# Performance work log

Hardware: AMD Instinct MI355X
Metric: run time of the kernel (lower is better)

The kernel has to match this reference:

```python
import jax, jax.numpy as jnp
import numpy as np

GROUP = 64      # int4 quantization group size
QMAX = 7.0      # symmetric int4 grid [-8, 7], scales from max/7
EPS = 1e-6      # RMSNorm epsilon


def fake_quant_int4(t, group=GROUP):
    """Symmetric per-group int4 fake-quantization along the last dim (STE)."""
    shp = t.shape
    g = t.reshape(shp[:-1] + (shp[-1] // group, group))
    s = jnp.maximum(jnp.max(jnp.abs(g), axis=-1, keepdims=True) / QMAX, 1e-8)
    q = jnp.clip(jnp.round(g / s), -8.0, 7.0) * s
    out = g + jax.lax.stop_gradient(q - g)  # straight-through
    return out.reshape(shp)


def rms_norm(x, w):
    var = jnp.mean(jnp.square(x), axis=-1, keepdims=True)
    return x * jax.lax.rsqrt(var + EPS) * w


def apply_rope(x, cos, sin):
    # x: [B,S,H,D]; cos/sin: [S, D//2]; rotate consecutive pairs (complex mult)
    xr = x.reshape(x.shape[:-1] + (x.shape[-1] // 2, 2))
    a, b = xr[..., 0], xr[..., 1]
    c = cos[None, :, None, :]
    s = sin[None, :, None, :]
    out = jnp.stack([a * c - b * s, a * s + b * c], axis=-1)
    return out.reshape(x.shape)


def setup_inputs() -> dict:
    B, S, C, OUT, R, D = 2, 4096, 3072, 9216, 32, 128
    key = jax.random.key(0)
    ks = jax.random.split(key, 6)
    x = jax.random.normal(ks[0], (B, S, C), jnp.float32)
    smooth = jax.random.uniform(ks[1], (C,), jnp.float32, minval=0.5, maxval=1.5)
    weight = jax.random.normal(ks[2], (OUT, C), jnp.float32) * 0.02
    proj_down = jax.random.normal(ks[3], (C, R), jnp.float32) * 0.02
    proj_up = jax.random.normal(ks[4], (OUT, R), jnp.float32) * 0.02
    bias = jax.random.normal(ks[5], (OUT,), jnp.float32) * 0.01
    norm_q_weight = jnp.ones((D,), jnp.float32)
    norm_k_weight = jnp.ones((D,), jnp.float32)
    half = D // 2
    inv_freq = 1.0 / (10000.0 ** (jnp.arange(half, dtype=jnp.float32) / half))
    ang = jnp.arange(S, dtype=jnp.float32)[:, None] * inv_freq[None, :]
    return {
        "x": x, "smooth": smooth, "weight": weight,
        "proj_down": proj_down, "proj_up": proj_up, "bias": bias,
        "norm_q_weight": norm_q_weight, "norm_k_weight": norm_k_weight,
        "freqs_cos": jnp.cos(ang), "freqs_sin": jnp.sin(ang),
    }


def reference(x, smooth, weight, proj_down, proj_up, bias,
              norm_q_weight, norm_k_weight, freqs_cos, freqs_sin):
    B, S, C = x.shape
    OUT = weight.shape[0]
    D = norm_q_weight.shape[0]
    H = (OUT // 3) // D
    # --- svdq_quantize_w4a4_act_fuse_lora: smooth, lora-down, int4 quantize ---
    xs = x.reshape(B * S, C) / smooth                 # smoothed activations
    lora_act = xs @ proj_down                          # [BS, R]
    xq = fake_quant_int4(xs)                           # per-token group-64 int4
    # --- svdq_gemm_w4a4: int4 GEMM + LoRA-up + bias epilogue ---
    wq = fake_quant_int4(weight)                       # per-row group-64 int4
    out = xq @ wq.T + lora_act @ proj_up.T + bias      # [BS, OUT]
    out = out.reshape(B, S, 3, H, D)                   # q,k,v concat order
    q, k, v = out[:, :, 0], out[:, :, 1], out[:, :, 2]
    # --- fused RMSNorm + RoPE epilogue on q and k ---
    q = apply_rope(rms_norm(q, norm_q_weight), freqs_cos, freqs_sin)
    k = apply_rope(rms_norm(k, norm_k_weight), freqs_cos, freqs_sin)
    return jnp.concatenate(
        [q.reshape(B, S, -1), k.reshape(B, S, -1), v.reshape(B, S, -1)], axis=-1)
```

## Files before the change

kernel.cpp:

```cpp
#include <hip/hip_runtime.h>

#define CDIM  3072
#define MROWS 8192
#define NOUT  9216
#define NTI   48

typedef __bf16 bf16x8 __attribute__((ext_vector_type(8)));
typedef float f32x4 __attribute__((ext_vector_type(4)));
typedef int i32x4 __attribute__((ext_vector_type(4)));

__device__ __forceinline__ unsigned short f2bf(float f) {
  union { float f; unsigned int u; } v; v.f = f;
  unsigned int u = v.u;
  return (unsigned short)((u + 0x7fffu + ((u >> 16) & 1u)) >> 16);
}
__device__ __forceinline__ float bfu_lo(unsigned int u) {
  union { unsigned int v; float f; } x; x.v = u << 16; return x.f;
}
__device__ __forceinline__ float bfu_hi(unsigned int u) {
  union { unsigned int v; float f; } x; x.v = u & 0xffff0000u; return x.f;
}
__device__ __forceinline__ void gld16(const void* g, void* l) {
  __builtin_amdgcn_global_load_lds(
      (const __attribute__((address_space(1))) void*)g,
      (__attribute__((address_space(3))) void*)l, 16, 0, 0);
}

#define BARRIER() asm volatile("s_barrier" ::: "memory")

template<int N> __device__ __forceinline__ void vmw() {
  if constexpr (N == 4)      asm volatile("s_waitcnt vmcnt(4)" ::: "memory");
  else if constexpr (N == 0) asm volatile("s_waitcnt vmcnt(0)" ::: "memory");
}

__device__ __forceinline__ unsigned int requant4(unsigned int u, float f) {
  const int q0 = (int)(signed char)(u & 0xff);
  const int q1 = (int)(signed char)((u >> 8) & 0xff);
  const int q2 = (int)(signed char)((u >> 16) & 0xff);
  const int q3 = (int)(signed char)(u >> 24);
  const int r0 = (int)rintf((float)q0 * f);
  const int r1 = (int)rintf((float)q1 * f);
  const int r2 = (int)rintf((float)q2 * f);
  const int r3 = (int)rintf((float)q3 * f);
  return (r0 & 0xff) | ((r1 & 0xff) << 8) | ((r2 & 0xff) << 16)
       | ((unsigned int)(r3 & 0xff) << 24);
}

__global__ __launch_bounds__(256) void k_prep(
    const float* __restrict__ wt, const float* __restrict__ pu,
    const float* __restrict__ x, const float* __restrict__ smooth,
    const float* __restrict__ pd,
    signed char* __restrict__ Bq, float* __restrict__ Sb_r,
    unsigned short* __restrict__ Blor,
    signed char* __restrict__ Aq, float* __restrict__ Sa_r,
    unsigned short* __restrict__ Alor) {
  __shared__ unsigned short xsb[4][3072];
  __shared__ float plds[4][32][33];
  __shared__ float sred[4];
  const int tid = threadIdx.x;

  if (blockIdx.x < NOUT) {
    const int row = blockIdx.x;
    unsigned int u[3]; float sl[3];
    #pragma unroll
    for (int it = 0; it < 3; ++it) {
      const int c = it * 1024 + tid * 4;
      const float4 v = *(const float4*)&wt[(size_t)row * CDIM + c];
      float am = fmaxf(fmaxf(fabsf(v.x), fabsf(v.y)), fmaxf(fabsf(v.z), fabsf(v.w)));
      #pragma unroll
      for (int off = 1; off < 16; off <<= 1) am = fmaxf(am, __shfl_xor(am, off));
      const float s = fmaxf(am / 7.0f, 1e-8f);
      union { signed char c[4]; unsigned int u; } pk;
      pk.c[0] = (signed char)(int)fminf(fmaxf(rintf(v.x / s), -8.f), 7.f);
      pk.c[1] = (signed char)(int)fminf(fmaxf(rintf(v.y / s), -8.f), 7.f);
      pk.c[2] = (signed char)(int)fminf(fmaxf(rintf(v.z / s), -8.f), 7.f);
      pk.c[3] = (signed char)(int)fminf(fmaxf(rintf(v.w / s), -8.f), 7.f);
      u[it] = pk.u; sl[it] = s;
    }
    float smax = fmaxf(fmaxf(sl[0], sl[1]), sl[2]);
    #pragma unroll
    for (int off = 16; off < 64; off <<= 1) smax = fmaxf(smax, __shfl_xor(smax, off));
    if ((tid & 63) == 0) sred[tid >> 6] = smax;
    __syncthreads();
    const float S = fmaxf(fmaxf(sred[0], sred[1]), fmaxf(sred[2], sred[3]));
    const float inv16 = 16.0f / S;
    #pragma unroll
    for (int it = 0; it < 3; ++it) {
      const int c = it * 1024 + tid * 4;
      *(unsigned int*)&Bq[(size_t)row * CDIM + c] = requant4(u[it], sl[it] * inv16);
    }
    if (tid == 0) Sb_r[row] = S * 0.0625f;
    if (tid < 32) Blor[row * 32 + tid] = f2bf(pu[row * 32 + tid]);
    return;
  }

  const int blk = blockIdx.x - NOUT;
  const int w = tid >> 6, l = tid & 63;
  const int row = blk * 4 + w;
  const float* xr = x + (size_t)row * CDIM;
  unsigned int u[12]; float sl[12];

  #pragma unroll
  for (int it = 0; it < 12; ++it) {
    const int c = it * 256 + l * 4;
    const float4 xv = *(const float4*)&xr[c];
    const float4 sm = *(const float4*)&smooth[c];
    float4 xs;
    xs.x = xv.x / sm.x; xs.y = xv.y / sm.y;
    xs.z = xv.z / sm.z; xs.w = xv.w / sm.w;
    ushort4 xb;
    xb.x = f2bf(xs.x); xb.y = f2bf(xs.y); xb.z = f2bf(xs.z); xb.w = f2bf(xs.w);
    *(ushort4*)&xsb[w][c] = xb;
    float am = fmaxf(fmaxf(fabsf(xs.x), fabsf(xs.y)), fmaxf(fabsf(xs.z), fabsf(xs.w)));
    #pragma unroll
    for (int off = 1; off < 16; off <<= 1) am = fmaxf(am, __shfl_xor(am, off));
    const float s = fmaxf(am / 7.0f, 1e-8f);
    union { signed char c[4]; unsigned int u; } pk;
    pk.c[0] = (signed char)(int)fminf(fmaxf(rintf(xs.x / s), -8.f), 7.f);
    pk.c[1] = (signed char)(int)fminf(fmaxf(rintf(xs.y / s), -8.f), 7.f);
    pk.c[2] = (signed char)(int)fminf(fmaxf(rintf(xs.z / s), -8.f), 7.f);
    pk.c[3] = (signed char)(int)fminf(fmaxf(rintf(xs.w / s), -8.f), 7.f);
    u[it] = pk.u; sl[it] = s;
  }
  float smax = sl[0];
  #pragma unroll
  for (int it = 1; it < 12; ++it) smax = fmaxf(smax, sl[it]);
  #pragma unroll
  for (int off = 16; off < 64; off <<= 1) smax = fmaxf(smax, __shfl_xor(smax, off));
  const float S = smax;
  const float inv16 = 16.0f / S;
  #pragma unroll
  for (int it = 0; it < 12; ++it) {
    const int c = it * 256 + l * 4;
    *(unsigned int*)&Aq[(size_t)row * CDIM + c] = requant4(u[it], sl[it] * inv16);
  }
  if (l == 0) Sa_r[row] = S * 0.0625f;
  __syncthreads();

  const int ch = tid >> 3, rg = tid & 7;
  float acc[4][4] = {};
  for (int i = 0; i < 48; ++i) {
    const int c = ch * 2 + i * 64;
    const float4 p0 = *(const float4*)&pd[(size_t)c * 32 + rg * 4];
    const float4 p1 = *(const float4*)&pd[(size_t)(c + 1) * 32 + rg * 4];
    #pragma unroll
    for (int r4 = 0; r4 < 4; ++r4) {
      const unsigned int uu = *(const unsigned int*)&xsb[r4][c];
      const float xa = bfu_lo(uu), xb = bfu_hi(uu);
      acc[r4][0] += xa * p0.x + xb * p1.x;
      acc[r4][1] += xa * p0.y + xb * p1.y;
      acc[r4][2] += xa * p0.z + xb * p1.z;
      acc[r4][3] += xa * p0.w + xb * p1.w;
    }
  }
  #pragma unroll
  for (int r4 = 0; r4 < 4; ++r4)
    #pragma unroll
    for (int jj = 0; jj < 4; ++jj)
      plds[r4][rg * 4 + jj][ch] = acc[r4][jj];
  __syncthreads();
  if (tid < 128) {
    const int rr = tid >> 5, r = tid & 31;
    float ssum = 0.f;
    #pragma unroll
    for (int cc = 0; cc < 32; ++cc) ssum += plds[rr][r][cc];
    Alor[(size_t)(blk * 4 + rr) * 32 + r] = f2bf(ssum);
  }
}

__global__ __launch_bounds__(256, 3) void k_gemmi8(
    const signed char* __restrict__ Aq, const signed char* __restrict__ Bq,
    const float* __restrict__ Sa_r, const float* __restrict__ Sb_r,
    const unsigned short* __restrict__ Alor, const unsigned short* __restrict__ Blor,
    const float* __restrict__ bias,
    const float* __restrict__ nqw, const float* __restrict__ nkw,
    const float* __restrict__ fcos, const float* __restrict__ fsin,
    float* __restrict__ outp) {
  __shared__ char lds[32768];
  const int tid = threadIdx.x;
  const int w = tid >> 6, l = tid & 63;
  const int wm = w >> 1, wn = w & 1;
  const int l16 = l & 15, g16 = l >> 4;
  const int xcd = blockIdx.x & 7;
  const int j = blockIdx.x >> 3;
  const int chunk = j / 36;
  const int t = j - chunk * 36;
  const int by = xcd * 8 + (chunk & 1) * 4 + t / 9;
  const int bx = (chunk >> 1) * 9 + t % 9;
  const int m0 = by * 128, n0 = bx * 128;
  const int fsb = (g16 ^ ((l16 >> 1) & 3)) << 4;
  const int rl = tid >> 2;
  const int swz = (((tid & 3) ^ ((rl >> 1) & 3)) << 4);
  const signed char* As0 = Aq + (size_t)(m0 + rl) * CDIM + swz;
  const signed char* As1 = As0 + (size_t)64 * CDIM;
  const signed char* Bs0 = Bq + (size_t)(n0 + rl) * CDIM + swz;
  const signed char* Bs1 = Bs0 + (size_t)64 * CDIM;

  i32x4 acc[4][4] = {};

  gld16(As0, lds + tid * 16);            gld16(As1, lds + 4096 + tid * 16);
  gld16(Bs0, lds + 8192 + tid * 16);     gld16(Bs1, lds + 8192 + 4096 + tid * 16);

  #pragma unroll 1
  for (int g = 0; g < NTI; ++g) {
    const int cb = (g & 1) * 16384;
    const int nb = ((g + 1) & 1) * 16384;
    if (g < NTI - 1) {
      const size_t kc = (size_t)(g + 1) * 64;
      gld16(As0 + kc, lds + nb + tid * 16);
      gld16(As1 + kc, lds + nb + 4096 + tid * 16);
      gld16(Bs0 + kc, lds + nb + 8192 + tid * 16);
      gld16(Bs1 + kc, lds + nb + 8192 + 4096 + tid * 16);
      vmw<4>();
    } else {
      vmw<0>();
    }
    BARRIER();
    i32x4 av[4], bv[4];
    #pragma unroll
    for (int mi = 0; mi < 4; ++mi)
      av[mi] = *(const i32x4*)(lds + cb + (wm * 64 + mi * 16 + l16) * 64 + fsb);
    #pragma unroll
    for (int ni = 0; ni < 4; ++ni)
      bv[ni] = *(const i32x4*)(lds + cb + 8192 + (wn * 64 + ni * 16 + l16) * 64 + fsb);
    __builtin_amdgcn_s_setprio(1);
    #pragma unroll
    for (int mi = 0; mi < 4; ++mi)
      #pragma unroll
      for (int ni = 0; ni < 4; ++ni)
        acc[mi][ni] = __builtin_amdgcn_mfma_i32_16x16x64_i8(av[mi], bv[ni], acc[mi][ni], 0, 0, 0);
    __builtin_amdgcn_s_setprio(0);
    BARRIER();
  }

  {
    const char* Al0 = (const char*)Alor + (size_t)(m0 + rl) * 64 + swz;
    const char* Bl0 = (const char*)Blor + (size_t)(n0 + rl) * 64 + swz;
    gld16(Al0, lds + tid * 16);            gld16(Al0 + 4096, lds + 4096 + tid * 16);
    gld16(Bl0, lds + 8192 + tid * 16);     gld16(Bl0 + 4096, lds + 8192 + 4096 + tid * 16);
  }

  f32x4 facc[4][4];
  float sbv[4];
  #pragma unroll
  for (int ni = 0; ni < 4; ++ni) sbv[ni] = Sb_r[n0 + wn * 64 + ni * 16 + l16];
  #pragma unroll
  for (int mi = 0; mi < 4; ++mi) {
    const f32x4 sa4 = *(const f32x4*)&Sa_r[m0 + wm * 64 + mi * 16 + g16 * 4];
    #pragma unroll
    for (int ni = 0; ni < 4; ++ni) {
      const f32x4 sab = sa4 * sbv[ni];
      facc[mi][ni] = __builtin_convertvector(acc[mi][ni], f32x4) * sab;
    }
  }

  vmw<0>();
  BARRIER();
  {
    bf16x8 bl[4];
    #pragma unroll
    for (int ni = 0; ni < 4; ++ni)
      bl[ni] = *(const bf16x8*)(lds + 8192 + (wn * 64 + ni * 16 + l16) * 64 + fsb);
    #pragma unroll
    for (int mi = 0; mi < 4; ++mi) {
      const bf16x8 al = *(const bf16x8*)(lds + (wm * 64 + mi * 16 + l16) * 64 + fsb);
      #pragma unroll
      for (int ni = 0; ni < 4; ++ni)
        facc[mi][ni] = __builtin_amdgcn_mfma_f32_16x16x32_bf16(al, bl[ni], facc[mi][ni], 0, 0, 0);
    }
  }

  float bvv[4];
  #pragma unroll
  for (int ni = 0; ni < 4; ++ni) bvv[ni] = bias[n0 + wn * 64 + ni * 16 + l16];
  #pragma unroll
  for (int mi = 0; mi < 4; ++mi)
    #pragma unroll
    for (int ni = 0; ni < 4; ++ni)
      #pragma unroll
      for (int jj = 0; jj < 4; ++jj) facc[mi][ni][jj] += bvv[ni];

  if (n0 < 6144) {
    const float* nwt = (n0 < 3072) ? nqw : nkw;
    float nw[4];
    #pragma unroll
    for (int ni = 0; ni < 4; ++ni) nw[ni] = nwt[wn * 64 + ni * 16 + l16];

    float part[4][4];
    #pragma unroll
    for (int mi = 0; mi < 4; ++mi)
      #pragma unroll
      for (int jj = 0; jj < 4; ++jj) {
        float ssum = 0.f;
        #pragma unroll
        for (int ni = 0; ni < 4; ++ni) ssum += facc[mi][ni][jj] * facc[mi][ni][jj];
        #pragma unroll
        for (int off = 1; off < 16; off <<= 1) ssum += __shfl_xor(ssum, off);
        part[mi][jj] = ssum;
      }

    __syncthreads();
    float* sq = (float*)lds;
    if (l16 == 0) {
      #pragma unroll
      for (int mi = 0; mi < 4; ++mi)
        #pragma unroll
        for (int jj = 0; jj < 4; ++jj)
          sq[(wm * 64 + mi * 16 + g16 * 4 + jj) * 2 + wn] = part[mi][jj];
    }
    __syncthreads();

    #pragma unroll
    for (int mi = 0; mi < 4; ++mi) {
      #pragma unroll
      for (int jj = 0; jj < 4; ++jj) {
        const int r128 = wm * 64 + mi * 16 + g16 * 4 + jj;
        const float other = sq[r128 * 2 + (wn ^ 1)];
        const float rinv = 1.0f / sqrtf((part[mi][jj] + other) * (1.0f / 128.0f) + 1e-6f);
        const int row = m0 + r128;
        const int sidx = row & 4095;
        #pragma unroll
        for (int ni = 0; ni < 4; ++ni) {
          const int p = wn * 32 + ni * 8 + (l16 >> 1);
          const float cv = fcos[(size_t)sidx * 64 + p];
          const float sv = fsin[(size_t)sidx * 64 + p];
          const float v = facc[mi][ni][jj] * rinv * nw[ni];
          const float o = __shfl_xor(v, 1);
          const float res = ((l & 1) == 0) ? (v * cv - o * sv) : (o * sv + v * cv);
          __builtin_nontemporal_store(res, &outp[(size_t)row * NOUT + n0 + wn * 64 + ni * 16 + l16]);
        }
      }
    }
  } else {
    #pragma unroll
    for (int ni = 0; ni < 4; ++ni) {
      const int gn = n0 + wn * 64 + ni * 16 + l16;
      #pragma unroll
      for (int mi = 0; mi < 4; ++mi) {
        const int gm = m0 + wm * 64 + mi * 16 + g16 * 4;
        #pragma unroll
        for (int jj = 0; jj < 4; ++jj)
          __builtin_nontemporal_store(facc[mi][ni][jj], &outp[(size_t)(gm + jj) * NOUT + gn]);
      }
    }
  }
}

extern "C" void kernel_launch(void* const* d_in, const int* in_sizes, int n_in,
                              void* d_out, int out_size, void* d_ws, size_t ws_size,
                              hipStream_t stream) {
  const float* x      = (const float*)d_in[0];
  const float* smooth = (const float*)d_in[1];
  const float* weight = (const float*)d_in[2];
  const float* pd     = (const float*)d_in[3];
  const float* pu     = (const float*)d_in[4];
  const float* bias   = (const float*)d_in[5];
  const float* nqw    = (const float*)d_in[6];
  const float* nkw    = (const float*)d_in[7];
  const float* fcos   = (const float*)d_in[8];
  const float* fsin   = (const float*)d_in[9];
  float* out = (float*)d_out;

  char* ws = (char*)d_ws;
  signed char* Aq   = (signed char*)ws;
  signed char* Bq   = (signed char*)(ws + 25165824);
  float* Sa_r       = (float*)(ws + 53477376);
  float* Sb_r       = (float*)(ws + 53510144);
  unsigned short* Alor = (unsigned short*)(ws + 53547008);
  unsigned short* Blor = (unsigned short*)(ws + 54071296);

  k_prep<<<dim3(NOUT + MROWS / 4), dim3(256), 0, stream>>>(
      weight, pu, x, smooth, pd, Bq, Sb_r, Blor, Aq, Sa_r, Alor);
  k_gemmi8<<<dim3(4608), dim3(256), 0, stream>>>(Aq, Bq, Sa_r, Sb_r, Alor, Blor,
                                                 bias, nqw, nkw, fcos, fsin, out);
}
```

Measured before the change: 419.7 us.

## Enlarge int8 GEMM tile to 256x256 with 8 waves and triple-buffered pipeline

Replaces the 128x128 tile with 4 waves by a 256x256 tile with 8 waves, each wave owning a 128x64 output region. The K loop is restructured into 128-wide windows split into four sub-steps whose A/B loads are interleaved with the MFMA phases over a three-stage LDS buffer of 128KB. The aim is higher arithmetic intensity per byte loaded and better overlap of global-to-LDS copies with compute. The cost is more LDS and registers per block, fewer resident blocks, and a more complex epilogue index mapping for the RMSNorm partial sums.

Result: faster. 369.2 us (-12.0%).

```diff
diff --git a/kernel.cpp b/kernel.cpp
--- a/kernel.cpp
+++ b/kernel.cpp
@@ -3,7 +3,7 @@
 #define CDIM  3072
 #define MROWS 8192
 #define NOUT  9216
-#define NTI   48
+#define NW    24
 
 typedef __bf16 bf16x8 __attribute__((ext_vector_type(8)));
 typedef float f32x4 __attribute__((ext_vector_type(4)));
@@ -27,9 +27,11 @@
 }
 
 #define BARRIER() asm volatile("s_barrier" ::: "memory")
+#define LGKM0()   asm volatile("s_waitcnt lgkmcnt(0)" ::: "memory")
 
 template<int N> __device__ __forceinline__ void vmw() {
-  if constexpr (N == 4)      asm volatile("s_waitcnt vmcnt(4)" ::: "memory");
+  if constexpr (N == 8)      asm volatile("s_waitcnt vmcnt(8)" ::: "memory");
+  else if constexpr (N == 4) asm volatile("s_waitcnt vmcnt(4)" ::: "memory");
   else if constexpr (N == 0) asm volatile("s_waitcnt vmcnt(0)" ::: "memory");
 }
 
@@ -168,7 +170,95 @@
   }
 }
 
-__global__ __launch_bounds__(256, 3) void k_gemmi8(
+template<int VM1, int VM3, int DO01, int DO23>
+__device__ __forceinline__ void gemm_window(
+    char* lds, i32x4 (&acc)[8][4],
+    const signed char* Asrc, const signed char* Bsrc,
+    int tid, int arow, int brow, int fsb, int par, int t) {
+  const int A0 = par * 16384;
+  const int A1 = 32768 + par * 16384;
+  const int B0 = 65536 + par * 16384;
+  const int B1 = 98304 + par * 16384;
+  const int A1n = 32768 + (par ^ 1) * 16384;
+  const int B1n = 98304 + (par ^ 1) * 16384;
+  i32x4 a[4], b[4];
+
+  #pragma unroll
+  for (int ni = 0; ni < 4; ++ni) b[ni] = *(const i32x4*)(lds + B0 + (brow + ni * 16) * 64 + fsb);
+  #pragma unroll
+  for (int mi = 0; mi < 4; ++mi) a[mi] = *(const i32x4*)(lds + A0 + (arow + mi * 16) * 64 + fsb);
+  if (DO01) {
+    const int kc = (t + 1) * 128 + 64;
+    gld16(Asrc + kc, lds + A1n + tid * 16);
+    gld16(Asrc + (size_t)128 * CDIM + kc, lds + A1n + 8192 + tid * 16);
+  }
+  BARRIER(); LGKM0();
+  __builtin_amdgcn_s_setprio(1);
+  #pragma unroll
+  for (int mi = 0; mi < 4; ++mi)
+    #pragma unroll
+    for (int ni = 0; ni < 4; ++ni)
+      acc[mi][ni] = __builtin_amdgcn_mfma_i32_16x16x64_i8(a[mi], b[ni], acc[mi][ni], 0, 0, 0);
+  __builtin_amdgcn_s_setprio(0);
+  BARRIER();
+
+  #pragma unroll
+  for (int mi = 0; mi < 4; ++mi) a[mi] = *(const i32x4*)(lds + A0 + (arow + 64 + mi * 16) * 64 + fsb);
+  if (DO01) {
+    const int kc = (t + 1) * 128 + 64;
+    gld16(Bsrc + kc, lds + B1n + tid * 16);
+    gld16(Bsrc + (size_t)128 * CDIM + kc, lds + B1n + 8192 + tid * 16);
+  }
+  BARRIER(); LGKM0();
+  __builtin_amdgcn_s_setprio(1);
+  #pragma unroll
+  for (int mi = 0; mi < 4; ++mi)
+    #pragma unroll
+    for (int ni = 0; ni < 4; ++ni)
+      acc[4 + mi][ni] = __builtin_amdgcn_mfma_i32_16x16x64_i8(a[mi], b[ni], acc[4 + mi][ni], 0, 0, 0);
+  __builtin_amdgcn_s_setprio(0);
+  vmw<VM1>();
+  BARRIER();
+
+  #pragma unroll
+  for (int ni = 0; ni < 4; ++ni) b[ni] = *(const i32x4*)(lds + B1 + (brow + ni * 16) * 64 + fsb);
+  #pragma unroll
+  for (int mi = 0; mi < 4; ++mi) a[mi] = *(const i32x4*)(lds + A1 + (arow + mi * 16) * 64 + fsb);
+  if (DO23) {
+    const int kc = (t + 2) * 128;
+    gld16(Asrc + kc, lds + A0 + tid * 16);
+    gld16(Asrc + (size_t)128 * CDIM + kc, lds + A0 + 8192 + tid * 16);
+  }
+  BARRIER(); LGKM0();
+  __builtin_amdgcn_s_setprio(1);
+  #pragma unroll
+  for (int mi = 0; mi < 4; ++mi)
+    #pragma unroll
+    for (int ni = 0; ni < 4; ++ni)
+      acc[mi][ni] = __builtin_amdgcn_mfma_i32_16x16x64_i8(a[mi], b[ni], acc[mi][ni], 0, 0, 0);
+  __builtin_amdgcn_s_setprio(0);
+  BARRIER();
+
+  #pragma unroll
+  for (int mi = 0; mi < 4; ++mi) a[mi] = *(const i32x4*)(lds + A1 + (arow + 64 + mi * 16) * 64 + fsb);
+  if (DO23) {
+    const int kc = (t + 2) * 128;
+    gld16(Bsrc + kc, lds + B0 + tid * 16);
+    gld16(Bsrc + (size_t)128 * CDIM + kc, lds + B0 + 8192 + tid * 16);
+  }
+  BARRIER(); LGKM0();
+  __builtin_amdgcn_s_setprio(1);
+  #pragma unroll
+  for (int mi = 0; mi < 4; ++mi)
+    #pragma unroll
+    for (int ni = 0; ni < 4; ++ni)
+      acc[4 + mi][ni] = __builtin_amdgcn_mfma_i32_16x16x64_i8(a[mi], b[ni], acc[4 + mi][ni], 0, 0, 0);
+  __builtin_amdgcn_s_setprio(0);
+  vmw<VM3>();
+  BARRIER();
+}
+
+__global__ __launch_bounds__(512, 2) void k_gemmi8(
     const signed char* __restrict__ Aq, const signed char* __restrict__ Bq,
     const float* __restrict__ Sa_r, const float* __restrict__ Sb_r,
     const unsigned short* __restrict__ Alor, const unsigned short* __restrict__ Blor,
@@ -176,171 +266,148 @@
     const float* __restrict__ nqw, const float* __restrict__ nkw,
     const float* __restrict__ fcos, const float* __restrict__ fsin,
     float* __restrict__ outp) {
-  __shared__ char lds[32768];
+  __shared__ char lds[131072];
   const int tid = threadIdx.x;
   const int w = tid >> 6, l = tid & 63;
-  const int wm = w >> 1, wn = w & 1;
+  const int wr = w >> 2, wc = w & 3;
   const int l16 = l & 15, g16 = l >> 4;
   const int xcd = blockIdx.x & 7;
-  const int j = blockIdx.x >> 3;
-  const int chunk = j / 36;
-  const int t = j - chunk * 36;
-  const int by = xcd * 8 + (chunk & 1) * 4 + t / 9;
-  const int bx = (chunk >> 1) * 9 + t % 9;
-  const int m0 = by * 128, n0 = bx * 128;
+  const int jj = blockIdx.x >> 3;
+  const int chunk = jj / 36;
+  const int tt = jj - chunk * 36;
+  const int by = xcd * 4 + tt / 9;
+  const int bx = chunk * 9 + tt % 9;
+  const int n0 = bx * 256, m0 = by * 256;
+  const int arow = wr * 128 + l16;
+  const int brow = wc * 64 + l16;
   const int fsb = (g16 ^ ((l16 >> 1) & 3)) << 4;
-  const int rl = tid >> 2;
-  const int swz = (((tid & 3) ^ ((rl >> 1) & 3)) << 4);
-  const signed char* As0 = Aq + (size_t)(m0 + rl) * CDIM + swz;
-  const signed char* As1 = As0 + (size_t)64 * CDIM;
-  const signed char* Bs0 = Bq + (size_t)(n0 + rl) * CDIM + swz;
-  const signed char* Bs1 = Bs0 + (size_t)64 * CDIM;
-
-  i32x4 acc[4][4] = {};
-
-  gld16(As0, lds + tid * 16);            gld16(As1, lds + 4096 + tid * 16);
-  gld16(Bs0, lds + 8192 + tid * 16);     gld16(Bs1, lds + 8192 + 4096 + tid * 16);
+  const int sr = tid >> 2;
+  const int ss = (((tid & 3) ^ ((sr >> 1) & 3)) << 4);
+  const signed char* Asrc = Aq + (size_t)(m0 + sr) * CDIM + ss;
+  const signed char* Bsrc = Bq + (size_t)(n0 + sr) * CDIM + ss;
+  i32x4 acc[8][4] = {};
+
+  gld16(Asrc, lds + tid * 16);                  gld16(Asrc + (size_t)128 * CDIM, lds + 8192 + tid * 16);
+  gld16(Bsrc, lds + 65536 + tid * 16);          gld16(Bsrc + (size_t)128 * CDIM, lds + 73728 + tid * 16);
+  gld16(Asrc + 64, lds + 32768 + tid * 16);     gld16(Asrc + (size_t)128 * CDIM + 64, lds + 40960 + tid * 16);
+  gld16(Bsrc + 64, lds + 98304 + tid * 16);     gld16(Bsrc + (size_t)128 * CDIM + 64, lds + 106496 + tid * 16);
+  gld16(Asrc + 128, lds + 16384 + tid * 16);    gld16(Asrc + (size_t)128 * CDIM + 128, lds + 24576 + tid * 16);
+  gld16(Bsrc + 128, lds + 81920 + tid * 16);    gld16(Bsrc + (size_t)128 * CDIM + 128, lds + 90112 + tid * 16);
+  vmw<8>(); BARRIER();
 
   #pragma unroll 1
-  for (int g = 0; g < NTI; ++g) {
-    const int cb = (g & 1) * 16384;
-    const int nb = ((g + 1) & 1) * 16384;
-    if (g < NTI - 1) {
-      const size_t kc = (size_t)(g + 1) * 64;
-      gld16(As0 + kc, lds + nb + tid * 16);
-      gld16(As1 + kc, lds + nb + 4096 + tid * 16);
-      gld16(Bs0 + kc, lds + nb + 8192 + tid * 16);
-      gld16(Bs1 + kc, lds + nb + 8192 + 4096 + tid * 16);
-      vmw<4>();
-    } else {
-      vmw<0>();
-    }
-    BARRIER();
-    i32x4 av[4], bv[4];
-    #pragma unroll
-    for (int mi = 0; mi < 4; ++mi)
-      av[mi] = *(const i32x4*)(lds + cb + (wm * 64 + mi * 16 + l16) * 64 + fsb);
-    #pragma unroll
-    for (int ni = 0; ni < 4; ++ni)
-      bv[ni] = *(const i32x4*)(lds + cb + 8192 + (wn * 64 + ni * 16 + l16) * 64 + fsb);
-    __builtin_amdgcn_s_setprio(1);
-    #pragma unroll
-    for (int mi = 0; mi < 4; ++mi)
-      #pragma unroll
-      for (int ni = 0; ni < 4; ++ni)
-        acc[mi][ni] = __builtin_amdgcn_mfma_i32_16x16x64_i8(av[mi], bv[ni], acc[mi][ni], 0, 0, 0);
-    __builtin_amdgcn_s_setprio(0);
-    BARRIER();
-  }
+  for (int t = 0; t <= NW - 3; ++t)
+    gemm_window<8, 8, 1, 1>(lds, acc, Asrc, Bsrc, tid, arow, brow, fsb, t & 1, t);
+  gemm_window<8, 4, 1, 0>(lds, acc, Asrc, Bsrc, tid, arow, brow, fsb, (NW - 2) & 1, NW - 2);
+  gemm_window<0, 63, 0, 0>(lds, acc, Asrc, Bsrc, tid, arow, brow, fsb, (NW - 1) & 1, NW - 1);
 
   {
-    const char* Al0 = (const char*)Alor + (size_t)(m0 + rl) * 64 + swz;
-    const char* Bl0 = (const char*)Blor + (size_t)(n0 + rl) * 64 + swz;
-    gld16(Al0, lds + tid * 16);            gld16(Al0 + 4096, lds + 4096 + tid * 16);
-    gld16(Bl0, lds + 8192 + tid * 16);     gld16(Bl0 + 4096, lds + 8192 + 4096 + tid * 16);
-  }
-
-  f32x4 facc[4][4];
+    const char* Al0 = (const char*)Alor + (size_t)(m0 + sr) * 64 + ss;
+    const char* Bl0 = (const char*)Blor + (size_t)(n0 + sr) * 64 + ss;
+    gld16(Al0, lds + tid * 16);            gld16(Al0 + 128 * 64, lds + 8192 + tid * 16);
+    gld16(Bl0, lds + 65536 + tid * 16);    gld16(Bl0 + 128 * 64, lds + 73728 + tid * 16);
+  }
+
+  f32x4 facc[8][4];
   float sbv[4];
   #pragma unroll
-  for (int ni = 0; ni < 4; ++ni) sbv[ni] = Sb_r[n0 + wn * 64 + ni * 16 + l16];
-  #pragma unroll
-  for (int mi = 0; mi < 4; ++mi) {
-    const f32x4 sa4 = *(const f32x4*)&Sa_r[m0 + wm * 64 + mi * 16 + g16 * 4];
-    #pragma unroll
-    for (int ni = 0; ni < 4; ++ni) {
-      const f32x4 sab = sa4 * sbv[ni];
-      facc[mi][ni] = __builtin_convertvector(acc[mi][ni], f32x4) * sab;
-    }
-  }
-
-  vmw<0>();
-  BARRIER();
+  for (int ni = 0; ni < 4; ++ni) sbv[ni] = Sb_r[n0 + wc * 64 + ni * 16 + l16];
+  #pragma unroll
+  for (int q = 0; q < 8; ++q) {
+    const f32x4 sa4 = *(const f32x4*)&Sa_r[m0 + wr * 128 + q * 16 + g16 * 4];
+    #pragma unroll
+    for (int ni = 0; ni < 4; ++ni)
+      facc[q][ni] = __builtin_convertvector(acc[q][ni], f32x4) * (sa4 * sbv[ni]);
+  }
+
+  vmw<0>(); BARRIER();
   {
     bf16x8 bl[4];
     #pragma unroll
     for (int ni = 0; ni < 4; ++ni)
-      bl[ni] = *(const bf16x8*)(lds + 8192 + (wn * 64 + ni * 16 + l16) * 64 + fsb);
-    #pragma unroll
-    for (int mi = 0; mi < 4; ++mi) {
-      const bf16x8 al = *(const bf16x8*)(lds + (wm * 64 + mi * 16 + l16) * 64 + fsb);
+      bl[ni] = *(const bf16x8*)(lds + 65536 + (brow + ni * 16) * 64 + fsb);
+    #pragma unroll
+    for (int q = 0; q < 8; ++q) {
+      const bf16x8 al = *(const bf16x8*)(lds + (arow + q * 16) * 64 + fsb);
       #pragma unroll
       for (int ni = 0; ni < 4; ++ni)
-        facc[mi][ni] = __builtin_amdgcn_mfma_f32_16x16x32_bf16(al, bl[ni], facc[mi][ni], 0, 0, 0);
+        facc[q][ni] = __builtin_amdgcn_mfma_f32_16x16x32_bf16(al, bl[ni], facc[q][ni], 0, 0, 0);
     }
   }
 
   float bvv[4];
   #pragma unroll
-  for (int ni = 0; ni < 4; ++ni) bvv[ni] = bias[n0 + wn * 64 + ni * 16 + l16];
-  #pragma unroll
-  for (int mi = 0; mi < 4; ++mi)
-    #pragma unroll
-    for (int ni = 0; ni < 4; ++ni)
-      #pragma unroll
-      for (int jj = 0; jj < 4; ++jj) facc[mi][ni][jj] += bvv[ni];
+  for (int ni = 0; ni < 4; ++ni) bvv[ni] = bias[n0 + wc * 64 + ni * 16 + l16];
+  #pragma unroll
+  for (int q = 0; q < 8; ++q)
+    #pragma unroll
+    for (int ni = 0; ni < 4; ++ni)
+      #pragma unroll
+      for (int j = 0; j < 4; ++j) facc[q][ni][j] += bvv[ni];
 
   if (n0 < 6144) {
     const float* nwt = (n0 < 3072) ? nqw : nkw;
     float nw[4];
     #pragma unroll
-    for (int ni = 0; ni < 4; ++ni) nw[ni] = nwt[wn * 64 + ni * 16 + l16];
-
-    float part[4][4];
-    #pragma unroll
-    for (int mi = 0; mi < 4; ++mi)
-      #pragma unroll
-      for (int jj = 0; jj < 4; ++jj) {
+    for (int ni = 0; ni < 4; ++ni) nw[ni] = nwt[(wc & 1) * 64 + ni * 16 + l16];
+
+    float part[8][4];
+    #pragma unroll
+    for (int q = 0; q < 8; ++q)
+      #pragma unroll
+      for (int j = 0; j < 4; ++j) {
         float ssum = 0.f;
         #pragma unroll
-        for (int ni = 0; ni < 4; ++ni) ssum += facc[mi][ni][jj] * facc[mi][ni][jj];
+        for (int ni = 0; ni < 4; ++ni) ssum += facc[q][ni][j] * facc[q][ni][j];
         #pragma unroll
         for (int off = 1; off < 16; off <<= 1) ssum += __shfl_xor(ssum, off);
-        part[mi][jj] = ssum;
+        part[q][j] = ssum;
       }
 
     __syncthreads();
     float* sq = (float*)lds;
     if (l16 == 0) {
       #pragma unroll
-      for (int mi = 0; mi < 4; ++mi)
+      for (int q = 0; q < 8; ++q)
         #pragma unroll
-        for (int jj = 0; jj < 4; ++jj)
-          sq[(wm * 64 + mi * 16 + g16 * 4 + jj) * 2 + wn] = part[mi][jj];
+        for (int j = 0; j < 4; ++j) {
+          const int r128 = q * 16 + g16 * 4 + j;
+          sq[(((wr * 128 + r128) * 2 + (wc >> 1)) * 2) + (wc & 1)] = part[q][j];
+        }
     }
     __syncthreads();
 
     #pragma unroll
-    for (int mi = 0; mi < 4; ++mi) {
-      #pragma unroll
-      for (int jj = 0; jj < 4; ++jj) {
-        const int r128 = wm * 64 + mi * 16 + g16 * 4 + jj;
-        const float other = sq[r128 * 2 + (wn ^ 1)];
-        const float rinv = 1.0f / sqrtf((part[mi][jj] + other) * (1.0f / 128.0f) + 1e-6f);
-        const int row = m0 + r128;
+    for (int q = 0; q < 8; ++q) {
+      #pragma unroll
+      for (int j = 0; j < 4; ++j) {
+        const int r128 = q * 16 + g16 * 4 + j;
+        const float other = sq[(((wr * 128 + r128) * 2 + (wc >> 1)) * 2) + ((wc & 1) ^ 1)];
+        const float rinv = 1.0f / sqrtf((part[q][j] + other) * (1.0f / 128.0f) + 1e-6f);
+        const int row = m0 + wr * 128 + r128;
         const int sidx = row & 4095;
         #pragma unroll
         for (int ni = 0; ni < 4; ++ni) {
-          const int p = wn * 32 + ni * 8 + (l16 >> 1);
+          const int p = (wc & 1) * 32 + ni * 8 + (l16 >> 1);
           const float cv = fcos[(size_t)sidx * 64 + p];
           const float sv = fsin[(size_t)sidx * 64 + p];
-          const float v = facc[mi][ni][jj] * rinv * nw[ni];
+          const float v = facc[q][ni][j] * rinv * nw[ni];
           const float o = __shfl_xor(v, 1);
           const float res = ((l & 1) == 0) ? (v * cv - o * sv) : (o * sv + v * cv);
-          __builtin_nontemporal_store(res, &outp[(size_t)row * NOUT + n0 + wn * 64 + ni * 16 + l16]);
+          __builtin_nontemporal_store(res, &outp[(size_t)row * NOUT + n0 + wc * 64 + ni * 16 + l16]);
         }
       }
     }
   } else {
     #pragma unroll
     for (int ni = 0; ni < 4; ++ni) {
-      const int gn = n0 + wn * 64 + ni * 16 + l16;
-      #pragma unroll
-      for (int mi = 0; mi < 4; ++mi) {
-        const int gm = m0 + wm * 64 + mi * 16 + g16 * 4;
+      const int gn = n0 + wc * 64 + ni * 16 + l16;
+      #pragma unroll
+      for (int q = 0; q < 8; ++q) {
+        const int gm = m0 + wr * 128 + q * 16 + g16 * 4;
         #pragma unroll
-        for (int jj = 0; jj < 4; ++jj)
-          __builtin_nontemporal_store(facc[mi][ni][jj], &outp[(size_t)(gm + jj) * NOUT + gn]);
+        for (int j = 0; j < 4; ++j)
+          __builtin_nontemporal_store(facc[q][ni][j], &outp[(size_t)(gm + j) * NOUT + gn]);
       }
     }
   }
@@ -371,6 +438,6 @@
 
   k_prep<<<dim3(NOUT + MROWS / 4), dim3(256), 0, stream>>>(
       weight, pu, x, smooth, pd, Bq, Sb_r, Blor, Aq, Sa_r, Alor);
-  k_gemmi8<<<dim3(4608), dim3(256), 0, stream>>>(Aq, Bq, Sa_r, Sb_r, Alor, Blor,
+  k_gemmi8<<<dim3(1152), dim3(512), 0, stream>>>(Aq, Bq, Sa_r, Sb_r, Alor, Blor,
                                                  bias, nqw, nkw, fcos, fsin, out);
 }
```
